# Kernel tuning notes

Hardware: AMD Instinct MI355X
Metric: run time of the kernel (lower is better)

## Reference

```python
import jax, jax.numpy as jnp
import numpy as np

H = 2048      # hidden_size
C = 256       # controller_hidden
B = 8192      # batch (tokens)
DT = 0.1


def setup_inputs() -> dict:
    key = jax.random.key(0)
    ks = jax.random.split(key, 8)
    h = jax.random.normal(ks[0], (B, H), dtype=jnp.float32)
    v = jax.random.normal(ks[1], (B, H), dtype=jnp.float32)
    # controller_in: Linear(2H -> C)
    W_in = jax.random.normal(ks[2], (C, 2 * H), dtype=jnp.float32) / np.sqrt(2 * H)
    b_in = jax.random.normal(ks[3], (C,), dtype=jnp.float32) * 0.01
    # controller_out: Linear(C -> 3H), weight ~ N(0, 0.01); bias init [2.2, -2.2, 0.0] per split
    W_out = jax.random.normal(ks[4], (3 * H, C), dtype=jnp.float32) * 0.01
    b_out = jnp.concatenate([
        jnp.full((H,), 2.2, dtype=jnp.float32),
        jnp.full((H,), -2.2, dtype=jnp.float32),
        jnp.zeros((H,), dtype=jnp.float32),
    ])
    # mu_proj: Linear(H -> H, bias=False); init zeros in module, use small random for a non-trivial baseline
    W_mu = jax.random.normal(ks[5], (H, H), dtype=jnp.float32) * 0.01
    mu = jnp.zeros((H,), dtype=jnp.float32)
    return {"h": h, "v": v, "W_in": W_in, "b_in": b_in, "W_out": W_out,
            "b_out": b_out, "W_mu": W_mu, "mu": mu}


def reference(h, v, W_in, b_in, W_out, b_out, W_mu, mu):
    hv = jnp.concatenate([h, v], axis=-1)                    # [B, 2H]
    ctrl = jax.nn.silu(hv @ W_in.T + b_in)                   # [B, C]
    ctrl_out = ctrl @ W_out.T + b_out                        # [B, 3H]
    alpha_raw, beta_raw, gate_raw = jnp.split(ctrl_out, 3, axis=-1)
    alpha = jax.nn.sigmoid(alpha_raw)
    beta = jnp.minimum(jax.nn.softplus(beta_raw), 2.0)
    gate = jax.nn.sigmoid(gate_raw)
    mu_contextual = mu + h @ W_mu.T                          # [B, H]
    error = h - mu_contextual
    v_next = jnp.clip(alpha * v - beta * error, -10.0, 10.0)
    h_next = h + DT * gate * v_next
    return h_next, v_next, mu_contextual
```

## Files before the change

### kernel.cpp

```cpp
#include <hip/hip_runtime.h>
#include <cstdint>
#include <cstddef>

#define B_TOK 8192
#define HDIM  2048
#define CDIM  256
#define KHV   4096
#define N3H   6144
#define DT_C  0.1f

typedef __bf16 bf16x8 __attribute__((ext_vector_type(8)));
typedef float  f32x4  __attribute__((ext_vector_type(4)));

typedef __attribute__((address_space(1))) void as1_void;
typedef __attribute__((address_space(3))) void as3_void;

__device__ __forceinline__ void g2l16(const void* g, void* l) {
    __builtin_amdgcn_global_load_lds((as1_void*)(void*)(uintptr_t)(g),
                                     (as3_void*)l, 16, 0, 0);
}

__device__ __forceinline__ unsigned short f2bf(float f) {
    unsigned int u = __float_as_uint(f);
    u += 0x7fffu + ((u >> 16) & 1u);
    return (unsigned short)(u >> 16);
}

__device__ __forceinline__ float bf2f(unsigned short s) {
    return __uint_as_float((unsigned int)s << 16);
}

__device__ __forceinline__ float fsigmoid(float x) {
    return __builtin_amdgcn_rcpf(1.f + __expf(-x));
}
__device__ __forceinline__ float fsoftplus(float x) {
    float t = __expf(-fabsf(x));
    return fmaxf(x, 0.f) + 0.69314718056f * __log2f(1.f + t);
}

__global__ void k_convert(const float* __restrict__ hp, const float* __restrict__ vp,
                          const float* __restrict__ Win, const float* __restrict__ Wout,
                          const float* __restrict__ Wmu,
                          ushort4* __restrict__ hv_b, ushort4* __restrict__ Wmu_b,
                          ushort4* __restrict__ Wout_b, ushort4* __restrict__ Win_b)
{
    const int HV_V   = B_TOK * KHV / 4;
    const int WMU_V  = HDIM * HDIM / 4;
    const int WOUT_V = N3H * CDIM / 4;
    const int WIN_V  = CDIM * KHV / 4;
    const int TOT    = HV_V + WMU_V + WOUT_V + WIN_V;
    for (int i = blockIdx.x * blockDim.x + threadIdx.x; i < TOT;
         i += gridDim.x * blockDim.x) {
        float4 x;
        ushort4* dst;
        if (i < HV_V) {
            int b  = i >> 10;
            int c4 = i & 1023;
            x = (c4 < 512) ? ((const float4*)hp)[b * 512 + c4]
                           : ((const float4*)vp)[b * 512 + (c4 - 512)];
            dst = hv_b + i;
        } else if (i < HV_V + WMU_V) {
            int j = i - HV_V;
            x = ((const float4*)Wmu)[j];
            dst = Wmu_b + j;
        } else if (i < HV_V + WMU_V + WOUT_V) {
            int j = i - (HV_V + WMU_V);
            x = ((const float4*)Wout)[j];
            dst = Wout_b + j;
        } else {
            int j = i - (HV_V + WMU_V + WOUT_V);
            x = ((const float4*)Win)[j];
            dst = Win_b + j;
        }
        ushort4 o;
        o.x = f2bf(x.x); o.y = f2bf(x.y); o.z = f2bf(x.z); o.w = f2bf(x.w);
        *dst = o;
    }
}

__global__ __launch_bounds__(256, 2)
void k_gemm1(const unsigned short* __restrict__ A,
             const unsigned short* __restrict__ Bw,
             const float* __restrict__ b_in,
             unsigned short* __restrict__ ctrl)
{
    __shared__ unsigned short sA[64 * 32];
    __shared__ unsigned short sB[64 * 32];
    const int tid  = threadIdx.x;
    const int wid  = tid >> 6;
    const int lane = tid & 63;
    const int quad = lane >> 4;
    const int l15  = lane & 15;
    const int wm   = wid >> 1, wn = wid & 1;
    const int bm   = blockIdx.x * 64;
    const int bn   = blockIdx.y * 64;
    const int srow = lane >> 2;
    const int sk   = (lane & 3) * 8;

    f32x4 acc[2][2];
#pragma unroll
    for (int a = 0; a < 2; ++a)
#pragma unroll
        for (int b = 0; b < 2; ++b) acc[a][b] = (f32x4){0.f, 0.f, 0.f, 0.f};

    const unsigned short* Ag = A  + (size_t)(bm + wid * 16 + srow) * KHV + sk;
    const unsigned short* Bg = Bw + (size_t)(bn + wid * 16 + srow) * KHV + sk;
    unsigned short* lA = &sA[(wid * 16) * 32];
    unsigned short* lB = &sB[(wid * 16) * 32];

    for (int kt = 0; kt < KHV; kt += 32) {
        g2l16(Ag + kt, lA);
        g2l16(Bg + kt, lB);
        __syncthreads();
        bf16x8 aF[2], bF[2];
#pragma unroll
        for (int t = 0; t < 2; ++t)
            aF[t] = *(const bf16x8*)&sA[(wm * 32 + t * 16 + l15) * 32 + quad * 8];
#pragma unroll
        for (int t = 0; t < 2; ++t)
            bF[t] = *(const bf16x8*)&sB[(wn * 32 + t * 16 + l15) * 32 + quad * 8];
#pragma unroll
        for (int tm = 0; tm < 2; ++tm)
#pragma unroll
            for (int tn = 0; tn < 2; ++tn)
                acc[tm][tn] = __builtin_amdgcn_mfma_f32_16x16x32_bf16(
                    aF[tm], bF[tn], acc[tm][tn], 0, 0, 0);
        __syncthreads();
    }

#pragma unroll
    for (int tm = 0; tm < 2; ++tm)
#pragma unroll
        for (int tn = 0; tn < 2; ++tn) {
            const int n = bn + wn * 32 + tn * 16 + l15;
            const float bias = b_in[n];
#pragma unroll
            for (int r = 0; r < 4; ++r) {
                const int m = bm + wm * 32 + tm * 16 + quad * 4 + r;
                float x = acc[tm][tn][r] + bias;
                float s = x * fsigmoid(x);
                ctrl[(size_t)m * CDIM + n] = f2bf(s);
            }
        }
}

__global__ __launch_bounds__(256, 2)
void k_gemm3(const unsigned short* __restrict__ A,
             const unsigned short* __restrict__ Bw,
             const float* __restrict__ mu,
             float* __restrict__ outmu)
{
    __shared__ unsigned short sA[128 * 32];
    __shared__ unsigned short sB[128 * 32];
    const int tid  = threadIdx.x;
    const int wid  = tid >> 6;
    const int lane = tid & 63;
    const int quad = lane >> 4;
    const int l15  = lane & 15;
    const int wm   = wid >> 1, wn = wid & 1;
    const int bm   = blockIdx.x * 128;
    const int bn   = blockIdx.y * 128;
    const int srow = lane >> 2;
    const int sk   = (lane & 3) * 8;

    f32x4 acc[4][4];
#pragma unroll
    for (int a = 0; a < 4; ++a)
#pragma unroll
        for (int b = 0; b < 4; ++b) acc[a][b] = (f32x4){0.f, 0.f, 0.f, 0.f};

    const unsigned short* Ag0 = A  + (size_t)(bm + wid * 16 + srow) * KHV + sk;
    const unsigned short* Ag1 = A  + (size_t)(bm + (wid + 4) * 16 + srow) * KHV + sk;
    const unsigned short* Bg0 = Bw + (size_t)(bn + wid * 16 + srow) * HDIM + sk;
    const unsigned short* Bg1 = Bw + (size_t)(bn + (wid + 4) * 16 + srow) * HDIM + sk;
    unsigned short* lA0 = &sA[(wid * 16) * 32];
    unsigned short* lA1 = &sA[((wid + 4) * 16) * 32];
    unsigned short* lB0 = &sB[(wid * 16) * 32];
    unsigned short* lB1 = &sB[((wid + 4) * 16) * 32];

    for (int kt = 0; kt < HDIM; kt += 32) {
        g2l16(Ag0 + kt, lA0);
        g2l16(Ag1 + kt, lA1);
        g2l16(Bg0 + kt, lB0);
        g2l16(Bg1 + kt, lB1);
        __syncthreads();
        bf16x8 aF[4], bF[4];
#pragma unroll
        for (int t = 0; t < 4; ++t)
            aF[t] = *(const bf16x8*)&sA[(wm * 64 + t * 16 + l15) * 32 + quad * 8];
#pragma unroll
        for (int t = 0; t < 4; ++t)
            bF[t] = *(const bf16x8*)&sB[(wn * 64 + t * 16 + l15) * 32 + quad * 8];
#pragma unroll
        for (int tm = 0; tm < 4; ++tm)
#pragma unroll
            for (int tn = 0; tn < 4; ++tn)
                acc[tm][tn] = __builtin_amdgcn_mfma_f32_16x16x32_bf16(
                    aF[tm], bF[tn], acc[tm][tn], 0, 0, 0);
        __syncthreads();
    }

#pragma unroll
    for (int tm = 0; tm < 4; ++tm)
#pragma unroll
        for (int tn = 0; tn < 4; ++tn) {
            const int n = bn + wn * 64 + tn * 16 + l15;
            const float mub = mu[n];
#pragma unroll
            for (int r = 0; r < 4; ++r) {
                const int m = bm + wm * 64 + tm * 16 + quad * 4 + r;
                outmu[(size_t)m * HDIM + n] = acc[tm][tn][r] + mub;
            }
        }
}

__global__ __launch_bounds__(256, 4)
void k_gemm2(const unsigned short* __restrict__ A,
             const unsigned short* __restrict__ Bw,
             const float* __restrict__ b_out,
             const unsigned short* __restrict__ hv,
             const float* __restrict__ mu_ctx,
             float* __restrict__ outp)
{
    __shared__ unsigned short sA[64 * 32];
    __shared__ unsigned short sB[3][64 * 32];
    const int tid  = threadIdx.x;
    const int wid  = tid >> 6;
    const int lane = tid & 63;
    const int quad = lane >> 4;
    const int l15  = lane & 15;
    const int wm   = wid >> 1, wn = wid & 1;
    const int bm   = blockIdx.x * 64;
    const int bn   = blockIdx.y * 64;
    const int srow = lane >> 2;
    const int sk   = (lane & 3) * 8;

    f32x4 acc[3][2][2];
#pragma unroll
    for (int p = 0; p < 3; ++p)
#pragma unroll
        for (int a = 0; a < 2; ++a)
#pragma unroll
            for (int b = 0; b < 2; ++b) acc[p][a][b] = (f32x4){0.f, 0.f, 0.f, 0.f};

    const unsigned short* Ag  = A + (size_t)(bm + wid * 16 + srow) * CDIM + sk;
    const unsigned short* Bg0 = Bw + (size_t)(0 * HDIM + bn + wid * 16 + srow) * CDIM + sk;
    const unsigned short* Bg1 = Bw + (size_t)(1 * HDIM + bn + wid * 16 + srow) * CDIM + sk;
    const unsigned short* Bg2 = Bw + (size_t)(2 * HDIM + bn + wid * 16 + srow) * CDIM + sk;
    unsigned short* lA  = &sA[(wid * 16) * 32];
    unsigned short* lB0 = &sB[0][(wid * 16) * 32];
    unsigned short* lB1 = &sB[1][(wid * 16) * 32];
    unsigned short* lB2 = &sB[2][(wid * 16) * 32];

    for (int kt = 0; kt < CDIM; kt += 32) {
        g2l16(Ag  + kt, lA);
        g2l16(Bg0 + kt, lB0);
        g2l16(Bg1 + kt, lB1);
        g2l16(Bg2 + kt, lB2);
        __syncthreads();
        bf16x8 aF[2], bF[3][2];
#pragma unroll
        for (int t = 0; t < 2; ++t)
            aF[t] = *(const bf16x8*)&sA[(wm * 32 + t * 16 + l15) * 32 + quad * 8];
#pragma unroll
        for (int p = 0; p < 3; ++p)
#pragma unroll
            for (int t = 0; t < 2; ++t)
                bF[p][t] = *(const bf16x8*)&sB[p][(wn * 32 + t * 16 + l15) * 32 + quad * 8];
#pragma unroll
        for (int p = 0; p < 3; ++p)
#pragma unroll
            for (int tm = 0; tm < 2; ++tm)
#pragma unroll
                for (int tn = 0; tn < 2; ++tn)
                    acc[p][tm][tn] = __builtin_amdgcn_mfma_f32_16x16x32_bf16(
                        aF[tm], bF[p][tn], acc[p][tm][tn], 0, 0, 0);
        __syncthreads();
    }

#pragma unroll
    for (int tm = 0; tm < 2; ++tm)
#pragma unroll
        for (int tn = 0; tn < 2; ++tn) {
            const int i  = bn + wn * 32 + tn * 16 + l15;
            const float ba = b_out[i];
            const float bb = b_out[HDIM + i];
            const float bg = b_out[2 * HDIM + i];
#pragma unroll
            for (int r = 0; r < 4; ++r) {
                const int m = bm + wm * 32 + tm * 16 + quad * 4 + r;
                const size_t off = (size_t)m * HDIM + i;
                const float araw = acc[0][tm][tn][r] + ba;
                const float braw = acc[1][tm][tn][r] + bb;
                const float graw = acc[2][tm][tn][r] + bg;
                const float alpha = fsigmoid(araw);
                const float beta  = fminf(fsoftplus(braw), 2.f);
                const float gate  = fsigmoid(graw);
                const float hh = bf2f(hv[(size_t)m * KHV + i]);
                const float vv = bf2f(hv[(size_t)m * KHV + HDIM + i]);
                const float mm = mu_ctx[off];
                const float err = hh - mm;
                float vn = alpha * vv - beta * err;
                vn = fminf(fmaxf(vn, -10.f), 10.f);
                const float hn = hh + DT_C * gate * vn;
                outp[off] = hn;
                outp[(size_t)B_TOK * HDIM + off] = vn;
            }
        }
}

extern "C" void kernel_launch(void* const* d_in, const int* in_sizes, int n_in,
                              void* d_out, int out_size, void* d_ws, size_t ws_size,
                              hipStream_t stream)
{
    const float* hp    = (const float*)d_in[0];
    const float* vp    = (const float*)d_in[1];
    const float* Win   = (const float*)d_in[2];
    const float* b_in  = (const float*)d_in[3];
    const float* Wout  = (const float*)d_in[4];
    const float* b_out = (const float*)d_in[5];
    const float* Wmu   = (const float*)d_in[6];
    const float* mu    = (const float*)d_in[7];
    float* outp = (float*)d_out;

    char* ws = (char*)d_ws;
    size_t off = 0;
    unsigned short* hv_b   = (unsigned short*)(ws + off); off += (size_t)B_TOK * KHV * 2;
    unsigned short* Wmu_b  = (unsigned short*)(ws + off); off += (size_t)HDIM * HDIM * 2;
    unsigned short* Wout_b = (unsigned short*)(ws + off); off += (size_t)N3H * CDIM * 2;
    unsigned short* Win_b  = (unsigned short*)(ws + off); off += (size_t)CDIM * KHV * 2;
    unsigned short* ctrl   = (unsigned short*)(ws + off); off += (size_t)B_TOK * CDIM * 2;

    k_convert<<<dim3(4096), dim3(256), 0, stream>>>(
        hp, vp, Win, Wout, Wmu,
        (ushort4*)hv_b, (ushort4*)Wmu_b, (ushort4*)Wout_b, (ushort4*)Win_b);

    k_gemm1<<<dim3(128, 4), dim3(256), 0, stream>>>(hv_b, Win_b, b_in, ctrl);

    k_gemm3<<<dim3(64, 16), dim3(256), 0, stream>>>(
        hv_b, Wmu_b, mu, outp + (size_t)2 * B_TOK * HDIM);

    k_gemm2<<<dim3(128, 32), dim3(256), 0, stream>>>(
        ctrl, Wout_b, b_out, hv_b,
        outp + (size_t)2 * B_TOK * HDIM, outp);
}
```

Before: 523.7 us.

## Split-K the controller-input GEMM into four partials with a separate reduction kernel

The first GEMM (8192x256, K=4096) now runs as four K-slices of 1024, launched as a 3D grid with the N-tile index on x, so 2048 blocks run instead of 512. Each slice writes fp32 partials to a new workspace buffer. A new elementwise kernel sums the four partials, adds the bias, applies SiLU and writes bf16 ctrl. The aim is better CU occupancy for this small-N GEMM and better L2 reuse of the A rows across N-tiles, at the cost of 32 MB of extra partial-sum traffic and one more launch. The launch_bounds hints were also removed from gemm1 and gemm3.

```diff
diff --git a/kernel.cpp b/kernel.cpp
--- a/kernel.cpp
+++ b/kernel.cpp
@@ -78,11 +78,9 @@
     }
 }
 
-__global__ __launch_bounds__(256, 2)
-void k_gemm1(const unsigned short* __restrict__ A,
-             const unsigned short* __restrict__ Bw,
-             const float* __restrict__ b_in,
-             unsigned short* __restrict__ ctrl)
+__global__ void k_gemm1(const unsigned short* __restrict__ A,
+                        const unsigned short* __restrict__ Bw,
+                        float* __restrict__ ctrl_p)
 {
     __shared__ unsigned short sA[64 * 32];
     __shared__ unsigned short sB[64 * 32];
@@ -92,8 +90,10 @@
     const int quad = lane >> 4;
     const int l15  = lane & 15;
     const int wm   = wid >> 1, wn = wid & 1;
-    const int bm   = blockIdx.x * 64;
-    const int bn   = blockIdx.y * 64;
+    const int bn   = blockIdx.x * 64;
+    const int bm   = blockIdx.y * 64;
+    const int ks   = blockIdx.z;
+    const int k0   = ks * 1024;
     const int srow = lane >> 2;
     const int sk   = (lane & 3) * 8;
 
@@ -108,7 +108,7 @@
     unsigned short* lA = &sA[(wid * 16) * 32];
     unsigned short* lB = &sB[(wid * 16) * 32];
 
-    for (int kt = 0; kt < KHV; kt += 32) {
+    for (int kt = k0; kt < k0 + 1024; kt += 32) {
         g2l16(Ag + kt, lA);
         g2l16(Bg + kt, lB);
         __syncthreads();
@@ -128,27 +128,51 @@
         __syncthreads();
     }
 
+    float* outp = ctrl_p + (size_t)ks * B_TOK * CDIM;
 #pragma unroll
     for (int tm = 0; tm < 2; ++tm)
 #pragma unroll
         for (int tn = 0; tn < 2; ++tn) {
             const int n = bn + wn * 32 + tn * 16 + l15;
-            const float bias = b_in[n];
 #pragma unroll
             for (int r = 0; r < 4; ++r) {
                 const int m = bm + wm * 32 + tm * 16 + quad * 4 + r;
-                float x = acc[tm][tn][r] + bias;
-                float s = x * fsigmoid(x);
-                ctrl[(size_t)m * CDIM + n] = f2bf(s);
+                outp[(size_t)m * CDIM + n] = acc[tm][tn][r];
             }
         }
 }
 
-__global__ __launch_bounds__(256, 2)
-void k_gemm3(const unsigned short* __restrict__ A,
-             const unsigned short* __restrict__ Bw,
-             const float* __restrict__ mu,
-             float* __restrict__ outmu)
+__global__ void k_red(const float* __restrict__ ctrl_p,
+                      const float* __restrict__ b_in,
+                      ushort4* __restrict__ ctrl)
+{
+    const int TOT = B_TOK * CDIM / 4;
+    const int P   = B_TOK * CDIM / 4;
+    int i = blockIdx.x * blockDim.x + threadIdx.x;
+    if (i >= TOT) return;
+    const float4* p = (const float4*)ctrl_p;
+    float4 s0 = p[i];
+    float4 s1 = p[P + i];
+    float4 s2 = p[2 * P + i];
+    float4 s3 = p[3 * P + i];
+    const int n4 = i & 63;
+    float4 bb = ((const float4*)b_in)[n4];
+    float x0 = s0.x + s1.x + s2.x + s3.x + bb.x;
+    float x1 = s0.y + s1.y + s2.y + s3.y + bb.y;
+    float x2 = s0.z + s1.z + s2.z + s3.z + bb.z;
+    float x3 = s0.w + s1.w + s2.w + s3.w + bb.w;
+    ushort4 o;
+    o.x = f2bf(x0 * fsigmoid(x0));
+    o.y = f2bf(x1 * fsigmoid(x1));
+    o.z = f2bf(x2 * fsigmoid(x2));
+    o.w = f2bf(x3 * fsigmoid(x3));
+    ctrl[i] = o;
+}
+
+__global__ void k_gemm3(const unsigned short* __restrict__ A,
+                        const unsigned short* __restrict__ Bw,
+                        const float* __restrict__ mu,
+                        float* __restrict__ outmu)
 {
     __shared__ unsigned short sA[128 * 32];
     __shared__ unsigned short sB[128 * 32];
@@ -330,12 +354,14 @@
     unsigned short* Wout_b = (unsigned short*)(ws + off); off += (size_t)N3H * CDIM * 2;
     unsigned short* Win_b  = (unsigned short*)(ws + off); off += (size_t)CDIM * KHV * 2;
     unsigned short* ctrl   = (unsigned short*)(ws + off); off += (size_t)B_TOK * CDIM * 2;
+    float*          ctrl_p = (float*)(ws + off);          off += (size_t)4 * B_TOK * CDIM * 4;
 
     k_convert<<<dim3(4096), dim3(256), 0, stream>>>(
         hp, vp, Win, Wout, Wmu,
         (ushort4*)hv_b, (ushort4*)Wmu_b, (ushort4*)Wout_b, (ushort4*)Win_b);
 
-    k_gemm1<<<dim3(128, 4), dim3(256), 0, stream>>>(hv_b, Win_b, b_in, ctrl);
+    k_gemm1<<<dim3(4, 128, 4), dim3(256), 0, stream>>>(hv_b, Win_b, ctrl_p);
+    k_red<<<dim3(2048), dim3(256), 0, stream>>>(ctrl_p, b_in, (ushort4*)ctrl);
 
     k_gemm3<<<dim3(64, 16), dim3(256), 0, stream>>>(
         hv_b, Wmu_b, mu, outp + (size_t)2 * B_TOK * HDIM);
```

New measurement: 545.6 us. 1.04x slower.

## Merge gemm1 and gemm3 into one launch with block-index dispatch

Applied to the files above, without the earlier changes.

Combines the controller-input GEMM (hv·W_in, 512 blocks of 64x64) and the mu projection GEMM (h·W_mu, 1024 blocks of 128x128) into one kernel. Block index picks the branch, so the two independent GEMMs run concurrently across the GPU. This removes a kernel boundary and lets the small, underfilled gemm1 overlap with gemm3's work. In exchange, both branches share the larger LDS allocation and the register budget of the bigger tile, which may lower occupancy for the gemm1 blocks.

```diff
diff --git a/kernel.cpp b/kernel.cpp
--- a/kernel.cpp
+++ b/kernel.cpp
@@ -79,76 +79,13 @@
 }
 
 __global__ __launch_bounds__(256, 2)
-void k_gemm1(const unsigned short* __restrict__ A,
-             const unsigned short* __restrict__ Bw,
-             const float* __restrict__ b_in,
-             unsigned short* __restrict__ ctrl)
-{
-    __shared__ unsigned short sA[64 * 32];
-    __shared__ unsigned short sB[64 * 32];
-    const int tid  = threadIdx.x;
-    const int wid  = tid >> 6;
-    const int lane = tid & 63;
-    const int quad = lane >> 4;
-    const int l15  = lane & 15;
-    const int wm   = wid >> 1, wn = wid & 1;
-    const int bm   = blockIdx.x * 64;
-    const int bn   = blockIdx.y * 64;
-    const int srow = lane >> 2;
-    const int sk   = (lane & 3) * 8;
-
-    f32x4 acc[2][2];
-#pragma unroll
-    for (int a = 0; a < 2; ++a)
-#pragma unroll
-        for (int b = 0; b < 2; ++b) acc[a][b] = (f32x4){0.f, 0.f, 0.f, 0.f};
-
-    const unsigned short* Ag = A  + (size_t)(bm + wid * 16 + srow) * KHV + sk;
-    const unsigned short* Bg = Bw + (size_t)(bn + wid * 16 + srow) * KHV + sk;
-    unsigned short* lA = &sA[(wid * 16) * 32];
-    unsigned short* lB = &sB[(wid * 16) * 32];
-
-    for (int kt = 0; kt < KHV; kt += 32) {
-        g2l16(Ag + kt, lA);
-        g2l16(Bg + kt, lB);
-        __syncthreads();
-        bf16x8 aF[2], bF[2];
-#pragma unroll
-        for (int t = 0; t < 2; ++t)
-            aF[t] = *(const bf16x8*)&sA[(wm * 32 + t * 16 + l15) * 32 + quad * 8];
-#pragma unroll
-        for (int t = 0; t < 2; ++t)
-            bF[t] = *(const bf16x8*)&sB[(wn * 32 + t * 16 + l15) * 32 + quad * 8];
-#pragma unroll
-        for (int tm = 0; tm < 2; ++tm)
-#pragma unroll
-            for (int tn = 0; tn < 2; ++tn)
-                acc[tm][tn] = __builtin_amdgcn_mfma_f32_16x16x32_bf16(
-                    aF[tm], bF[tn], acc[tm][tn], 0, 0, 0);
-        __syncthreads();
-    }
-
-#pragma unroll
-    for (int tm = 0; tm < 2; ++tm)
-#pragma unroll
-        for (int tn = 0; tn < 2; ++tn) {
-            const int n = bn + wn * 32 + tn * 16 + l15;
-            const float bias = b_in[n];
-#pragma unroll
-            for (int r = 0; r < 4; ++r) {
-                const int m = bm + wm * 32 + tm * 16 + quad * 4 + r;
-                float x = acc[tm][tn][r] + bias;
-                float s = x * fsigmoid(x);
-                ctrl[(size_t)m * CDIM + n] = f2bf(s);
-            }
-        }
-}
-
-__global__ __launch_bounds__(256, 2)
-void k_gemm3(const unsigned short* __restrict__ A,
-             const unsigned short* __restrict__ Bw,
-             const float* __restrict__ mu,
-             float* __restrict__ outmu)
+void k_mid(const unsigned short* __restrict__ hvb,
+           const unsigned short* __restrict__ Winb,
+           const unsigned short* __restrict__ Wmub,
+           const float* __restrict__ b_in,
+           const float* __restrict__ mu,
+           unsigned short* __restrict__ ctrl,
+           float* __restrict__ outmu)
 {
     __shared__ unsigned short sA[128 * 32];
     __shared__ unsigned short sB[128 * 32];
@@ -158,60 +95,113 @@
     const int quad = lane >> 4;
     const int l15  = lane & 15;
     const int wm   = wid >> 1, wn = wid & 1;
-    const int bm   = blockIdx.x * 128;
-    const int bn   = blockIdx.y * 128;
     const int srow = lane >> 2;
     const int sk   = (lane & 3) * 8;
 
-    f32x4 acc[4][4];
-#pragma unroll
-    for (int a = 0; a < 4; ++a)
-#pragma unroll
-        for (int b = 0; b < 4; ++b) acc[a][b] = (f32x4){0.f, 0.f, 0.f, 0.f};
-
-    const unsigned short* Ag0 = A  + (size_t)(bm + wid * 16 + srow) * KHV + sk;
-    const unsigned short* Ag1 = A  + (size_t)(bm + (wid + 4) * 16 + srow) * KHV + sk;
-    const unsigned short* Bg0 = Bw + (size_t)(bn + wid * 16 + srow) * HDIM + sk;
-    const unsigned short* Bg1 = Bw + (size_t)(bn + (wid + 4) * 16 + srow) * HDIM + sk;
-    unsigned short* lA0 = &sA[(wid * 16) * 32];
-    unsigned short* lA1 = &sA[((wid + 4) * 16) * 32];
-    unsigned short* lB0 = &sB[(wid * 16) * 32];
-    unsigned short* lB1 = &sB[((wid + 4) * 16) * 32];
-
-    for (int kt = 0; kt < HDIM; kt += 32) {
-        g2l16(Ag0 + kt, lA0);
-        g2l16(Ag1 + kt, lA1);
-        g2l16(Bg0 + kt, lB0);
-        g2l16(Bg1 + kt, lB1);
-        __syncthreads();
-        bf16x8 aF[4], bF[4];
-#pragma unroll
-        for (int t = 0; t < 4; ++t)
-            aF[t] = *(const bf16x8*)&sA[(wm * 64 + t * 16 + l15) * 32 + quad * 8];
-#pragma unroll
-        for (int t = 0; t < 4; ++t)
-            bF[t] = *(const bf16x8*)&sB[(wn * 64 + t * 16 + l15) * 32 + quad * 8];
+    if (blockIdx.x < 512) {
+        const int bm = (blockIdx.x >> 2) * 64;
+        const int bn = (blockIdx.x & 3) * 64;
+
+        f32x4 acc[2][2];
+#pragma unroll
+        for (int a = 0; a < 2; ++a)
+#pragma unroll
+            for (int b = 0; b < 2; ++b) acc[a][b] = (f32x4){0.f, 0.f, 0.f, 0.f};
+
+        const unsigned short* Ag = hvb  + (size_t)(bm + wid * 16 + srow) * KHV + sk;
+        const unsigned short* Bg = Winb + (size_t)(bn + wid * 16 + srow) * KHV + sk;
+        unsigned short* lA = &sA[(wid * 16) * 32];
+        unsigned short* lB = &sB[(wid * 16) * 32];
+
+        for (int kt = 0; kt < KHV; kt += 32) {
+            g2l16(Ag + kt, lA);
+            g2l16(Bg + kt, lB);
+            __syncthreads();
+            bf16x8 aF[2], bF[2];
+#pragma unroll
+            for (int t = 0; t < 2; ++t)
+                aF[t] = *(const bf16x8*)&sA[(wm * 32 + t * 16 + l15) * 32 + quad * 8];
+#pragma unroll
+            for (int t = 0; t < 2; ++t)
+                bF[t] = *(const bf16x8*)&sB[(wn * 32 + t * 16 + l15) * 32 + quad * 8];
+#pragma unroll
+            for (int tm = 0; tm < 2; ++tm)
+#pragma unroll
+                for (int tn = 0; tn < 2; ++tn)
+                    acc[tm][tn] = __builtin_amdgcn_mfma_f32_16x16x32_bf16(
+                        aF[tm], bF[tn], acc[tm][tn], 0, 0, 0);
+            __syncthreads();
+        }
+
+#pragma unroll
+        for (int tm = 0; tm < 2; ++tm)
+#pragma unroll
+            for (int tn = 0; tn < 2; ++tn) {
+                const int n = bn + wn * 32 + tn * 16 + l15;
+                const float bias = b_in[n];
+#pragma unroll
+                for (int r = 0; r < 4; ++r) {
+                    const int m = bm + wm * 32 + tm * 16 + quad * 4 + r;
+                    float x = acc[tm][tn][r] + bias;
+                    float s = x * fsigmoid(x);
+                    ctrl[(size_t)m * CDIM + n] = f2bf(s);
+                }
+            }
+    } else {
+        const int t3 = blockIdx.x - 512;
+        const int bm = (t3 & 63) * 128;
+        const int bn = (t3 >> 6) * 128;
+
+        f32x4 acc[4][4];
+#pragma unroll
+        for (int a = 0; a < 4; ++a)
+#pragma unroll
+            for (int b = 0; b < 4; ++b) acc[a][b] = (f32x4){0.f, 0.f, 0.f, 0.f};
+
+        const unsigned short* Ag0 = hvb  + (size_t)(bm + wid * 16 + srow) * KHV + sk;
+        const unsigned short* Ag1 = hvb  + (size_t)(bm + (wid + 4) * 16 + srow) * KHV + sk;
+        const unsigned short* Bg0 = Wmub + (size_t)(bn + wid * 16 + srow) * HDIM + sk;
+        const unsigned short* Bg1 = Wmub + (size_t)(bn + (wid + 4) * 16 + srow) * HDIM + sk;
+        unsigned short* lA0 = &sA[(wid * 16) * 32];
+        unsigned short* lA1 = &sA[((wid + 4) * 16) * 32];
+        unsigned short* lB0 = &sB[(wid * 16) * 32];
+        unsigned short* lB1 = &sB[((wid + 4) * 16) * 32];
+
+        for (int kt = 0; kt < HDIM; kt += 32) {
+            g2l16(Ag0 + kt, lA0);
+            g2l16(Ag1 + kt, lA1);
+            g2l16(Bg0 + kt, lB0);
+            g2l16(Bg1 + kt, lB1);
+            __syncthreads();
+            bf16x8 aF[4], bF[4];
+#pragma unroll
+            for (int t = 0; t < 4; ++t)
+                aF[t] = *(const bf16x8*)&sA[(wm * 64 + t * 16 + l15) * 32 + quad * 8];
+#pragma unroll
+            for (int t = 0; t < 4; ++t)
+                bF[t] = *(const bf16x8*)&sB[(wn * 64 + t * 16 + l15) * 32 + quad * 8];
+#pragma unroll
+            for (int tm = 0; tm < 4; ++tm)
+#pragma unroll
+                for (int tn = 0; tn < 4; ++tn)
+                    acc[tm][tn] = __builtin_amdgcn_mfma_f32_16x16x32_bf16(
+                        aF[tm], bF[tn], acc[tm][tn], 0, 0, 0);
+            __syncthreads();
+        }
+
 #pragma unroll
         for (int tm = 0; tm < 4; ++tm)
 #pragma unroll
-            for (int tn = 0; tn < 4; ++tn)
-                acc[tm][tn] = __builtin_amdgcn_mfma_f32_16x16x32_bf16(
-                    aF[tm], bF[tn], acc[tm][tn], 0, 0, 0);
-        __syncthreads();
+            for (int tn = 0; tn < 4; ++tn) {
+                const int n = bn + wn * 64 + tn * 16 + l15;
+                const float mub = mu[n];
+#pragma unroll
+                for (int r = 0; r < 4; ++r) {
+                    const int m = bm + wm * 64 + tm * 16 + quad * 4 + r;
+                    outmu[(size_t)m * HDIM + n] = acc[tm][tn][r] + mub;
+                }
+            }
     }
-
-#pragma unroll
-    for (int tm = 0; tm < 4; ++tm)
-#pragma unroll
-        for (int tn = 0; tn < 4; ++tn) {
-            const int n = bn + wn * 64 + tn * 16 + l15;
-            const float mub = mu[n];
-#pragma unroll
-            for (int r = 0; r < 4; ++r) {
-                const int m = bm + wm * 64 + tm * 16 + quad * 4 + r;
-                outmu[(size_t)m * HDIM + n] = acc[tm][tn][r] + mub;
-            }
-        }
 }
 
 __global__ __launch_bounds__(256, 4)
@@ -335,10 +325,8 @@
         hp, vp, Win, Wout, Wmu,
         (ushort4*)hv_b, (ushort4*)Wmu_b, (ushort4*)Wout_b, (ushort4*)Win_b);
 
-    k_gemm1<<<dim3(128, 4), dim3(256), 0, stream>>>(hv_b, Win_b, b_in, ctrl);
-
-    k_gemm3<<<dim3(64, 16), dim3(256), 0, stream>>>(
-        hv_b, Wmu_b, mu, outp + (size_t)2 * B_TOK * HDIM);
+    k_mid<<<dim3(1536), dim3(256), 0, stream>>>(
+        hv_b, Win_b, Wmu_b, b_in, mu, ctrl, outp + (size_t)2 * B_TOK * HDIM);
 
     k_gemm2<<<dim3(128, 32), dim3(256), 0, stream>>>(
         ctrl, Wout_b, b_out, hv_b,
```

Result: faster. 510.4 us (-2.5%).
